# Kernel tuning notes

Hardware: AMD Instinct MI355X
Metric: run time of the kernel (lower is better)

Reference implementation:

```python
import jax, jax.numpy as jnp
import numpy as np
import math

N_RES, N_EDGE = 10000, 320000
C_S, C_Z, C_H, H, PQ, PV = 384, 128, 16, 12, 4, 8
INF, EPS = 1e5, 1e-8


def _lin(key, din, dout):
    k1, k2 = jax.random.split(key)
    w = jax.random.normal(k1, (din, dout), jnp.float32) * (1.0 / np.sqrt(din))
    b = jax.random.normal(k2, (dout,), jnp.float32) * 0.02
    return w, b


def setup_inputs() -> dict:
    key = jax.random.key(0)
    ks = jax.random.split(key, 16)
    s = jax.random.normal(ks[0], (N_RES, C_S), jnp.float32)
    z = jax.random.normal(ks[1], (N_EDGE, C_Z), jnp.float32)
    edge_index = jax.random.randint(ks[2], (2, N_EDGE), 0, N_RES, jnp.int32)
    rot = jnp.linalg.qr(jax.random.normal(ks[3], (N_RES, 3, 3), jnp.float32))[0]
    trans = jax.random.normal(ks[4], (N_RES, 3), jnp.float32)
    mask = jnp.ones((N_RES,), jnp.float32)
    wq, bq = _lin(ks[5], C_S, H * C_H)
    wkv, bkv = _lin(ks[6], C_S, 2 * H * C_H)
    wqp, bqp = _lin(ks[7], C_S, H * PQ * 3)
    wkvp, bkvp = _lin(ks[8], C_S, H * (PQ + PV) * 3)
    wb, bb = _lin(ks[9], C_Z, H)
    wdz, bdz = _lin(ks[10], C_Z, C_Z // 4)
    head_w = jax.random.normal(ks[11], (H,), jnp.float32) * 0.1
    wout, bout = _lin(ks[12], H * (C_Z // 4 + C_H + PV * 4), C_S)
    return dict(s=s, z=z, rot=rot, trans=trans, mask=mask, edge_index=edge_index,
                wq=wq, bq=bq, wkv=wkv, bkv=bkv, wqp=wqp, bqp=bqp, wkvp=wkvp, bkvp=bkvp,
                wb=wb, bb=bb, wdz=wdz, bdz=bdz, head_w=head_w, wout=wout, bout=bout)


def reference(s, z, rot, trans, mask, edge_index, wq, bq, wkv, bkv, wqp, bqp,
              wkvp, bkvp, wb, bb, wdz, bdz, head_w, wout, bout):
    n = s.shape[0]
    src, dst = edge_index[0], edge_index[1]  # key-side, query-side

    q = (s @ wq + bq).reshape(n, H, C_H)
    kv = (s @ wkv + bkv).reshape(n, H, 2 * C_H)
    k, v = kv[..., :C_H], kv[..., C_H:]

    def make_pts(x, p):
        # torch: split [n, H*p*3] into 3 chunks of H*p, stack on last dim -> [n, H*p, 3]
        x = jnp.stack(jnp.split(x, 3, axis=-1), axis=-1)
        x = jnp.einsum('nij,npj->npi', rot, x) + trans[:, None, :]  # global frame
        return x.reshape(n, H, p, 3)

    q_pts = make_pts(s @ wqp + bqp, PQ)                 # [n, H, PQ, 3]
    kv_pts = make_pts(s @ wkvp + bkvp, PQ + PV)
    k_pts, v_pts = kv_pts[..., :PQ, :], kv_pts[..., PQ:, :]

    b = z @ wb + bb                                      # [E, H]
    a = jnp.einsum('ehc,ehc->eh', q[dst], k[src]) * math.sqrt(1.0 / (3 * C_H))
    a = a + math.sqrt(1.0 / 3) * b

    disp = q_pts[dst] - k_pts[src]                       # [E, H, PQ, 3]
    hw = jax.nn.softplus(head_w) * math.sqrt(1.0 / (3 * (PQ * 9.0 / 2)))
    pt_att = -0.5 * jnp.einsum('ehp,h->eh', jnp.sum(disp * disp, axis=-1), hw)

    edge_mask = INF * (mask[src] * mask[dst] - 1.0)
    a = a + pt_att + edge_mask[:, None]

    # segment softmax over edges grouped by destination node
    m = jax.lax.stop_gradient(jax.ops.segment_max(a, dst, num_segments=n))
    ea = jnp.exp(a - m[dst])
    a = ea / (jax.ops.segment_sum(ea, dst, num_segments=n)[dst] + 1e-16)

    o = jax.ops.segment_sum(a[..., None] * v[src], dst, num_segments=n).reshape(n, -1)

    o_pt = jax.ops.segment_sum(a[..., None, None] * v_pts[src], dst, num_segments=n)  # [n,H,PV,3]
    o_pt = jnp.einsum('nji,nhpj->nhpi', rot, o_pt - trans[:, None, None, :])  # invert_apply
    o_pt_norm = jnp.sqrt(jnp.sum(o_pt * o_pt, axis=-1) + EPS).reshape(n, -1)
    o_pt = o_pt.reshape(n, H * PV, 3)

    pair_z = z @ wdz + bdz                               # [E, c_z//4]
    o_pair = jax.ops.segment_sum(a[..., None] * pair_z[:, None, :], dst,
                                 num_segments=n).reshape(n, -1)

    feats = jnp.concatenate([o, o_pt[..., 0], o_pt[..., 1], o_pt[..., 2],
                             o_pt_norm, o_pair], axis=-1)
    return feats @ wout + bout
```

## Files before the change

### kernel.cpp

```cpp
#include <hip/hip_runtime.h>
#include <hip/hip_bf16.h>
#include <math.h>

#define N_RESC 10000
#define N_EDGEC 320000
#define C_SC 384
#define C_ZC 128
#define AGG_D 864
#define FEAT_D 960
#define OUT_D 384

#define S1C 0.14433756729740643f
#define S2C 0.5773502691896258f
#define SHWC 0.13608276348795434f

__global__ void k_zero(int* cursor) {
    int i = blockIdx.x * 256 + threadIdx.x;
    if (i < N_RESC) cursor[i] = 0;
}

__global__ void k_hist(const int* __restrict__ ei, int* cursor) {
    int e = blockIdx.x * 256 + threadIdx.x;
    if (e < N_EDGEC) atomicAdd(&cursor[ei[N_EDGEC + e]], 1);
}

__global__ __launch_bounds__(1024) void k_scan(int* cursor, int* rowptr) {
    __shared__ int buf[1024];
    __shared__ int carry_s;
    int t = threadIdx.x;
    if (t == 0) carry_s = 0;
    __syncthreads();
    for (int ch = 0; ch < 10; ++ch) {
        int idx = ch * 1024 + t;
        int v = (idx < N_RESC) ? cursor[idx] : 0;
        buf[t] = v;
        __syncthreads();
        for (int off = 1; off < 1024; off <<= 1) {
            int x = (t >= off) ? buf[t - off] : 0;
            __syncthreads();
            buf[t] += x;
            __syncthreads();
        }
        int incl = buf[t];
        int excl = incl - v;
        int base = carry_s;
        int total = buf[1023];
        if (idx < N_RESC) { rowptr[idx] = base + excl; cursor[idx] = base + excl; }
        __syncthreads();
        if (t == 0) carry_s = base + total;
        __syncthreads();
    }
    if (t == 0) rowptr[N_RESC] = carry_s;
}

__global__ void k_scatter(const int* __restrict__ ei, int* cursor, int* csr,
                          int* src_csr, int* epos) {
    int e = blockIdx.x * 256 + threadIdx.x;
    if (e < N_EDGEC) {
        int d = ei[N_EDGEC + e];
        int s = ei[e];
        int pos = atomicAdd(&cursor[d], 1);
        csr[pos] = e;
        src_csr[pos] = s;
        epos[e] = pos;
    }
}

__global__ __launch_bounds__(256) void k_wpack(
    const float* __restrict__ wq, const float* __restrict__ bq,
    const float* __restrict__ wkv, const float* __restrict__ bkv,
    const float* __restrict__ wqp, const float* __restrict__ bqp,
    const float* __restrict__ wkvp, const float* __restrict__ bkvp,
    const float* __restrict__ wb, const float* __restrict__ bb,
    const float* __restrict__ wdz, const float* __restrict__ bdz,
    float* __restrict__ wpack, float* __restrict__ bpack,
    float* __restrict__ wzpack, float* __restrict__ bzpack) {
    int idx = blockIdx.x * 256 + threadIdx.x;
    if (idx < 384 * 1152) {
        int j = idx / 1152, c = idx % 1152;
        float v;
        if (c < 192)      v = wq[j * 192 + c];
        else if (c < 576) v = wkv[j * 384 + (c - 192)];
        else if (c < 720) v = wqp[j * 144 + (c - 576)];
        else              v = wkvp[j * 432 + (c - 720)];
        wpack[idx] = v;
    }
    if (idx < 1152) {
        float b;
        if (idx < 192)      b = bq[idx];
        else if (idx < 576) b = bkv[idx - 192];
        else if (idx < 720) b = bqp[idx - 576];
        else                b = bkvp[idx - 720];
        bpack[idx] = b;
    }
    if (idx < 128 * 48) {
        int j = idx / 48, c = idx % 48;
        float v = 0.f;
        if (c < 12)      v = wb[j * 12 + c];
        else if (c < 44) v = wdz[j * 32 + (c - 12)];
        wzpack[idx] = v;
    }
    if (idx < 48) {
        float b = 0.f;
        if (idx < 12)      b = bb[idx];
        else if (idx < 44) b = bdz[idx - 12];
        bzpack[idx] = b;
    }
}

#define BM 64
#define BN 128
#define BK 32
__global__ __launch_bounds__(256) void k_proj(const float* __restrict__ s,
    const float* __restrict__ wpack, const float* __restrict__ bpack,
    float* __restrict__ qh, float* __restrict__ kh, float* __restrict__ vh,
    float* __restrict__ praw) {
    __shared__ float sT[BK][BM + 4];
    __shared__ float wt[BK][BN];
    int t = threadIdx.x;
    int bm0 = blockIdx.x * BM;
    int bn0 = blockIdx.y * BN;
    int tcol = t & 31;
    int trow = t >> 5;
    int c0 = tcol * 4;
    int r0 = trow * 8;

    int srow = t >> 2;
    int skoff = (t & 3) * 8;
    int gsrow = min(bm0 + srow, N_RESC - 1);
    const float* srcp = s + (long)gsrow * C_SC + skoff;

    float acc[8][4];
    #pragma unroll
    for (int i = 0; i < 8; i++)
        #pragma unroll
        for (int j = 0; j < 4; j++) acc[i][j] = 0.f;

    for (int k0 = 0; k0 < C_SC; k0 += BK) {
        float4 sa = *(const float4*)(srcp + k0);
        float4 sb = *(const float4*)(srcp + k0 + 4);
        sT[skoff + 0][srow] = sa.x; sT[skoff + 1][srow] = sa.y;
        sT[skoff + 2][srow] = sa.z; sT[skoff + 3][srow] = sa.w;
        sT[skoff + 4][srow] = sb.x; sT[skoff + 5][srow] = sb.y;
        sT[skoff + 6][srow] = sb.z; sT[skoff + 7][srow] = sb.w;
        #pragma unroll
        for (int q = 0; q < 4; q++) {
            int kk = (t >> 5) + q * 8;
            *(float4*)&wt[kk][c0] =
                *(const float4*)(wpack + (long)(k0 + kk) * 1152 + bn0 + c0);
        }
        __syncthreads();
        #pragma unroll
        for (int k = 0; k < BK; k++) {
            float4 a0 = *(const float4*)&sT[k][r0];
            float4 a1 = *(const float4*)&sT[k][r0 + 4];
            float4 b  = *(const float4*)&wt[k][c0];
            float av0 = a0.x, av1 = a0.y, av2 = a0.z, av3 = a0.w;
            float av4 = a1.x, av5 = a1.y, av6 = a1.z, av7 = a1.w;
            acc[0][0] = fmaf(av0, b.x, acc[0][0]); acc[0][1] = fmaf(av0, b.y, acc[0][1]);
            acc[0][2] = fmaf(av0, b.z, acc[0][2]); acc[0][3] = fmaf(av0, b.w, acc[0][3]);
            acc[1][0] = fmaf(av1, b.x, acc[1][0]); acc[1][1] = fmaf(av1, b.y, acc[1][1]);
            acc[1][2] = fmaf(av1, b.z, acc[1][2]); acc[1][3] = fmaf(av1, b.w, acc[1][3]);
            acc[2][0] = fmaf(av2, b.x, acc[2][0]); acc[2][1] = fmaf(av2, b.y, acc[2][1]);
            acc[2][2] = fmaf(av2, b.z, acc[2][2]); acc[2][3] = fmaf(av2, b.w, acc[2][3]);
            acc[3][0] = fmaf(av3, b.x, acc[3][0]); acc[3][1] = fmaf(av3, b.y, acc[3][1]);
            acc[3][2] = fmaf(av3, b.z, acc[3][2]); acc[3][3] = fmaf(av3, b.w, acc[3][3]);
            acc[4][0] = fmaf(av4, b.x, acc[4][0]); acc[4][1] = fmaf(av4, b.y, acc[4][1]);
            acc[4][2] = fmaf(av4, b.z, acc[4][2]); acc[4][3] = fmaf(av4, b.w, acc[4][3]);
            acc[5][0] = fmaf(av5, b.x, acc[5][0]); acc[5][1] = fmaf(av5, b.y, acc[5][1]);
            acc[5][2] = fmaf(av5, b.z, acc[5][2]); acc[5][3] = fmaf(av5, b.w, acc[5][3]);
            acc[6][0] = fmaf(av6, b.x, acc[6][0]); acc[6][1] = fmaf(av6, b.y, acc[6][1]);
            acc[6][2] = fmaf(av6, b.z, acc[6][2]); acc[6][3] = fmaf(av6, b.w, acc[6][3]);
            acc[7][0] = fmaf(av7, b.x, acc[7][0]); acc[7][1] = fmaf(av7, b.y, acc[7][1]);
            acc[7][2] = fmaf(av7, b.z, acc[7][2]); acc[7][3] = fmaf(av7, b.w, acc[7][3]);
        }
        __syncthreads();
    }
    #pragma unroll
    for (int j = 0; j < 4; j++) {
        int c = bn0 + c0 + j;
        float bv = bpack[c];
        #pragma unroll
        for (int i = 0; i < 8; i++) {
            int n = bm0 + r0 + i;
            if (n < N_RESC) {
                float val = acc[i][j] + bv;
                if (c < 192) qh[(long)n * 192 + c] = val;
                else if (c < 576) {
                    int cc = c - 192; int h = cc >> 5, r = cc & 31;
                    if (r < 16) kh[(long)n * 192 + h * 16 + r] = val;
                    else        vh[(long)n * 192 + h * 16 + (r - 16)] = val;
                } else praw[(long)n * 576 + (c - 576)] = val;
            }
        }
    }
}

__global__ __launch_bounds__(192) void k_rot(const float* __restrict__ praw,
    const float* __restrict__ rot, const float* __restrict__ trans,
    float* __restrict__ qpts, float* __restrict__ kpts, float* __restrict__ vpts) {
    int n = blockIdx.x;
    int t = threadIdx.x;
    __shared__ float R[9], T[3];
    if (t < 9) R[t] = rot[n * 9 + t];
    if (t < 3) T[t] = trans[n * 3 + t];
    __syncthreads();
    const float* pr = praw + (long)n * 576;
    if (t < 48) {
        float x0 = pr[t], x1 = pr[48 + t], x2 = pr[96 + t];
        #pragma unroll
        for (int i = 0; i < 3; i++)
            qpts[(long)n * 144 + t * 3 + i] = R[i*3+0]*x0 + R[i*3+1]*x1 + R[i*3+2]*x2 + T[i];
    } else {
        int p = t - 48;
        float x0 = pr[144 + p], x1 = pr[288 + p], x2 = pr[432 + p];
        int h = p / 12, pp = p % 12;
        #pragma unroll
        for (int i = 0; i < 3; i++) {
            float val = R[i*3+0]*x0 + R[i*3+1]*x1 + R[i*3+2]*x2 + T[i];
            if (pp < 4) kpts[(long)n * 144 + (h * 4 + pp) * 3 + i] = val;
            else        vpts[(long)n * 288 + (h * 8 + (pp - 4)) * 3 + i] = val;
        }
    }
}

#define ZBM 128
__global__ __launch_bounds__(256) void k_zproj(const float* __restrict__ z,
    const int* __restrict__ epos,
    const float* __restrict__ wzpack, const float* __restrict__ bzpack,
    float* __restrict__ b_e, float* __restrict__ pairz) {
    __shared__ float zT[32][ZBM + 4];
    __shared__ float wl[128][48];
    int t = threadIdx.x;
    long e0 = (long)blockIdx.x * ZBM;
    int er = t & 31;
    int cg = t >> 5;
    int cb = cg * 6;

    #pragma unroll
    for (int q = 0; q < 6; q++) {
        int f = t + q * 256;
        int row = f / 12, c4 = f % 12;
        *(float4*)&wl[row][c4 * 4] = *(const float4*)(wzpack + row * 48 + c4 * 4);
    }

    float acc[4][6];
    #pragma unroll
    for (int i = 0; i < 4; i++)
        #pragma unroll
        for (int j = 0; j < 6; j++) acc[i][j] = 0.f;

    int r = t >> 1, ch2 = t & 1;
    const float* zp = z + (e0 + r) * C_ZC + ch2 * 16;

    for (int kc = 0; kc < 4; kc++) {
        __syncthreads();
        #pragma unroll
        for (int q = 0; q < 4; q++) {
            float4 v = *(const float4*)(zp + kc * 32 + q * 4);
            int kk = ch2 * 16 + q * 4;
            zT[kk + 0][r] = v.x; zT[kk + 1][r] = v.y;
            zT[kk + 2][r] = v.z; zT[kk + 3][r] = v.w;
        }
        __syncthreads();
        #pragma unroll
        for (int k = 0; k < 32; k++) {
            float4 zv = *(const float4*)&zT[k][er * 4];
            const float* wrow = &wl[kc * 32 + k][cb];
            float w0 = wrow[0], w1 = wrow[1], w2 = wrow[2];
            float w3 = wrow[3], w4 = wrow[4], w5 = wrow[5];
            acc[0][0] = fmaf(zv.x, w0, acc[0][0]); acc[0][1] = fmaf(zv.x, w1, acc[0][1]);
            acc[0][2] = fmaf(zv.x, w2, acc[0][2]); acc[0][3] = fmaf(zv.x, w3, acc[0][3]);
            acc[0][4] = fmaf(zv.x, w4, acc[0][4]); acc[0][5] = fmaf(zv.x, w5, acc[0][5]);
            acc[1][0] = fmaf(zv.y, w0, acc[1][0]); acc[1][1] = fmaf(zv.y, w1, acc[1][1]);
            acc[1][2] = fmaf(zv.y, w2, acc[1][2]); acc[1][3] = fmaf(zv.y, w3, acc[1][3]);
            acc[1][4] = fmaf(zv.y, w4, acc[1][4]); acc[1][5] = fmaf(zv.y, w5, acc[1][5]);
            acc[2][0] = fmaf(zv.z, w0, acc[2][0]); acc[2][1] = fmaf(zv.z, w1, acc[2][1]);
            acc[2][2] = fmaf(zv.z, w2, acc[2][2]); acc[2][3] = fmaf(zv.z, w3, acc[2][3]);
            acc[2][4] = fmaf(zv.z, w4, acc[2][4]); acc[2][5] = fmaf(zv.z, w5, acc[2][5]);
            acc[3][0] = fmaf(zv.w, w0, acc[3][0]); acc[3][1] = fmaf(zv.w, w1, acc[3][1]);
            acc[3][2] = fmaf(zv.w, w2, acc[3][2]); acc[3][3] = fmaf(zv.w, w3, acc[3][3]);
            acc[3][4] = fmaf(zv.w, w4, acc[3][4]); acc[3][5] = fmaf(zv.w, w5, acc[3][5]);
        }
    }

    float bz0 = bzpack[cb + 0], bz1 = bzpack[cb + 1], bz2 = bzpack[cb + 2];
    float bz3 = bzpack[cb + 3], bz4 = bzpack[cb + 4], bz5 = bzpack[cb + 5];
    #pragma unroll
    for (int ei = 0; ei < 4; ei++) {
        long pos = epos[e0 + er * 4 + ei];
        float o0 = acc[ei][0] + bz0, o1 = acc[ei][1] + bz1;
        float o2 = acc[ei][2] + bz2, o3 = acc[ei][3] + bz3;
        float o4 = acc[ei][4] + bz4, o5 = acc[ei][5] + bz5;
        if (cb < 12) {
            float* d = b_e + pos * 12 + cb;
            *(float2*)(d + 0) = make_float2(o0, o1);
            *(float2*)(d + 2) = make_float2(o2, o3);
            *(float2*)(d + 4) = make_float2(o4, o5);
        } else if (cb < 42) {
            float* d = pairz + pos * 32 + (cb - 12);
            *(float2*)(d + 0) = make_float2(o0, o1);
            *(float2*)(d + 2) = make_float2(o2, o3);
            *(float2*)(d + 4) = make_float2(o4, o5);
        } else {
            *(float2*)(pairz + pos * 32 + 30) = make_float2(o0, o1);
        }
    }
}

#define CAPL 256
__global__ __launch_bounds__(256) void k_logit(const int* __restrict__ rowptr,
    const int* __restrict__ src_csr,
    const float* __restrict__ qh, const float* __restrict__ kh,
    const float* __restrict__ qpts, const float* __restrict__ kpts,
    const float* __restrict__ mask, const float* __restrict__ head_w,
    const float* __restrict__ b_e, float* __restrict__ alog) {
    int n = blockIdx.x;
    int t = threadIdx.x;
    __shared__ float qf[192], qp[144], hws[12];
    __shared__ int slist[CAPL];
    if (t < 192) qf[t] = qh[(long)n * 192 + t];
    if (t < 144) qp[t] = qpts[(long)n * 144 + t];
    if (t < 12)  hws[t] = log1pf(expf(head_w[t])) * SHWC;
    float mdst = mask[n];
    int row0 = rowptr[n];
    int deg = rowptr[n + 1] - row0;
    int w = t >> 6, l = t & 63, c = l & 15, hq = l >> 4;
    for (int cs = 0; cs < deg; cs += CAPL) {
        int cnt = min(CAPL, deg - cs);
        __syncthreads();
        for (int i = t; i < cnt; i += 256) slist[i] = src_csr[row0 + cs + i];
        __syncthreads();
        for (int i = w * 2; i < cnt; i += 8) {
            int i1 = min(i + 1, cnt - 1);
            int s0 = slist[i], s1 = slist[i1];
            int pos0 = row0 + cs + i, pos1 = row0 + cs + i1;
            float em0 = 100000.0f * (mask[s0] * mdst - 1.0f);
            float em1 = 100000.0f * (mask[s1] * mdst - 1.0f);
            float kv0[3], kv1[3];
            #pragma unroll
            for (int tp = 0; tp < 3; tp++) {
                kv0[tp] = kh[(long)s0 * 192 + tp * 64 + l];
                kv1[tp] = kh[(long)s1 * 192 + tp * 64 + l];
            }
            float kp0[3] = {0.f,0.f,0.f}, kp1[3] = {0.f,0.f,0.f};
            if (c < 12) {
                #pragma unroll
                for (int tp = 0; tp < 3; tp++) {
                    int h = tp * 4 + hq;
                    kp0[tp] = kpts[(long)s0 * 144 + h * 12 + c];
                    kp1[tp] = kpts[(long)s1 * 144 + h * 12 + c];
                }
            }
            float be0[3] = {0.f,0.f,0.f}, be1[3] = {0.f,0.f,0.f};
            if (c == 0) {
                #pragma unroll
                for (int tp = 0; tp < 3; tp++) {
                    int h = tp * 4 + hq;
                    be0[tp] = b_e[(long)pos0 * 12 + h];
                    be1[tp] = b_e[(long)pos1 * 12 + h];
                }
            }
            #pragma unroll
            for (int tp = 0; tp < 3; tp++) {
                int h = tp * 4 + hq;
                float qfv = S1C * qf[h * 16 + c];
                float val0 = qfv * kv0[tp];
                float val1 = qfv * kv1[tp];
                if (c < 12) {
                    float qpv = qp[h * 12 + c];
                    float hw = -0.5f * hws[h];
                    float d0 = qpv - kp0[tp];
                    float d1 = qpv - kp1[tp];
                    val0 = fmaf(hw * d0, d0, val0);
                    val1 = fmaf(hw * d1, d1, val1);
                }
                val0 += __shfl_xor(val0, 8, 16); val1 += __shfl_xor(val1, 8, 16);
                val0 += __shfl_xor(val0, 4, 16); val1 += __shfl_xor(val1, 4, 16);
                val0 += __shfl_xor(val0, 2, 16); val1 += __shfl_xor(val1, 2, 16);
                val0 += __shfl_xor(val0, 1, 16); val1 += __shfl_xor(val1, 1, 16);
                if (c == 0) {
                    alog[(long)pos0 * 12 + h] = val0 + S2C * be0[tp] + em0;
                    if (i1 != i)
                        alog[(long)pos1 * 12 + h] = val1 + S2C * be1[tp] + em1;
                }
            }
        }
    }
}

#define CAPE 256
__global__ __launch_bounds__(256) void k_agg(const int* __restrict__ rowptr,
    const int* __restrict__ src_csr,
    const float* __restrict__ alog, const float* __restrict__ vh,
    const float* __restrict__ vpts, const float* __restrict__ pairz,
    float* __restrict__ agg) {
    int n = blockIdx.x;
    int t = threadIdx.x;
    __shared__ float red[16 * 12];
    __shared__ float mh[12], linv[12];
    __shared__ float al[CAPE * 12];
    __shared__ int sl_[CAPE];
    int row0 = rowptr[n];
    int deg = rowptr[n + 1] - row0;
    int g = t >> 4, l16 = t & 15;
    if (l16 < 12) {
        float lm = -1e30f;
        for (int i = g; i < deg; i += 16)
            lm = fmaxf(lm, alog[(long)(row0 + i) * 12 + l16]);
        red[g * 12 + l16] = lm;
    }
    __syncthreads();
    if (t < 12) {
        float m = -1e30f;
        for (int gg = 0; gg < 16; gg++) m = fmaxf(m, red[gg * 12 + t]);
        mh[t] = m;
    }
    __syncthreads();
    if (l16 < 12) {
        float m = mh[l16];
        float ls = 0.f;
        for (int i = g; i < deg; i += 16)
            ls += expf(alog[(long)(row0 + i) * 12 + l16] - m);
        red[g * 12 + l16] = ls;
    }
    __syncthreads();
    if (t < 12) {
        float ssum = 0.f;
        for (int gg = 0; gg < 16; gg++) ssum += red[gg * 12 + t];
        linv[t] = 1.f / (ssum + 1e-16f);
    }

    const float* base = nullptr;
    int scale = 0, hk = 0, use_e = 0;
    int comp = t * 4;
    if (comp < 192)      { base = vh + comp; scale = 192; hk = comp >> 4; }
    else if (comp < 480) { int idx = comp - 192; base = vpts + idx; scale = 288; hk = idx / 24; }
    else if (comp < 864) { int idx = comp - 480; base = pairz + (idx & 31); scale = 32; hk = idx >> 5; use_e = 1; }
    float4 acc = make_float4(0.f, 0.f, 0.f, 0.f);

    for (int cs = 0; cs < deg; cs += CAPE) {
        int cnt = min(CAPE, deg - cs);
        int p0 = row0 + cs;
        __syncthreads();
        for (int i = t; i < cnt * 12; i += 256) {
            int h = i % 12;
            al[i] = expf(alog[(long)p0 * 12 + i] - mh[h]) * linv[h];
        }
        for (int i = t; i < cnt; i += 256) sl_[i] = src_csr[p0 + i];
        __syncthreads();
        if (t < 216) {
            int i = 0;
            for (; i + 4 <= cnt; i += 4) {
                int i0 = use_e ? (p0 + i)     : sl_[i];
                int i1 = use_e ? (p0 + i + 1) : sl_[i+1];
                int i2 = use_e ? (p0 + i + 2) : sl_[i+2];
                int i3 = use_e ? (p0 + i + 3) : sl_[i+3];
                float4 v0 = *(const float4*)(base + (long)i0 * scale);
                float4 v1 = *(const float4*)(base + (long)i1 * scale);
                float4 v2 = *(const float4*)(base + (long)i2 * scale);
                float4 v3 = *(const float4*)(base + (long)i3 * scale);
                float w0 = al[i * 12 + hk];
                float w1 = al[(i+1) * 12 + hk];
                float w2 = al[(i+2) * 12 + hk];
                float w3 = al[(i+3) * 12 + hk];
                acc.x = fmaf(w0, v0.x, acc.x); acc.y = fmaf(w0, v0.y, acc.y);
                acc.z = fmaf(w0, v0.z, acc.z); acc.w = fmaf(w0, v0.w, acc.w);
                acc.x = fmaf(w1, v1.x, acc.x); acc.y = fmaf(w1, v1.y, acc.y);
                acc.z = fmaf(w1, v1.z, acc.z); acc.w = fmaf(w1, v1.w, acc.w);
                acc.x = fmaf(w2, v2.x, acc.x); acc.y = fmaf(w2, v2.y, acc.y);
                acc.z = fmaf(w2, v2.z, acc.z); acc.w = fmaf(w2, v2.w, acc.w);
                acc.x = fmaf(w3, v3.x, acc.x); acc.y = fmaf(w3, v3.y, acc.y);
                acc.z = fmaf(w3, v3.z, acc.z); acc.w = fmaf(w3, v3.w, acc.w);
            }
            for (; i < cnt; i++) {
                int ii = use_e ? (p0 + i) : sl_[i];
                float4 v = *(const float4*)(base + (long)ii * scale);
                float w = al[i * 12 + hk];
                acc.x = fmaf(w, v.x, acc.x); acc.y = fmaf(w, v.y, acc.y);
                acc.z = fmaf(w, v.z, acc.z); acc.w = fmaf(w, v.w, acc.w);
            }
        }
    }
    if (t < 216) *(float4*)(agg + (long)n * AGG_D + comp) = acc;
}

#define NT_F 8
__global__ __launch_bounds__(192) void k_final(const float* __restrict__ agg,
    const float* __restrict__ rot, const float* __restrict__ trans,
    const float* __restrict__ wout, const float* __restrict__ bout,
    float* __restrict__ out) {
    __shared__ float f[NT_F][FEAT_D];
    int t = threadIdx.x;
    int node0 = blockIdx.x * NT_F;
    for (int idx = t; idx < NT_F * 192; idx += 192) {
        int nt = idx / 192, c = idx % 192;
        f[nt][c] = agg[(long)(node0 + nt) * AGG_D + c];
    }
    for (int idx = t; idx < NT_F * 96; idx += 192) {
        int nt = idx / 96, p = idx % 96;
        int n = node0 + nt;
        const float* a = agg + (long)n * AGG_D;
        float gx = a[192 + p * 3 + 0] - trans[n * 3 + 0];
        float gy = a[192 + p * 3 + 1] - trans[n * 3 + 1];
        float gz = a[192 + p * 3 + 2] - trans[n * 3 + 2];
        const float* R = rot + (long)n * 9;
        float lx = R[0] * gx + R[3] * gy + R[6] * gz;
        float ly = R[1] * gx + R[4] * gy + R[7] * gz;
        float lz = R[2] * gx + R[5] * gy + R[8] * gz;
        f[nt][192 + p] = lx;
        f[nt][288 + p] = ly;
        f[nt][384 + p] = lz;
        f[nt][480 + p] = sqrtf(lx * lx + ly * ly + lz * lz + 1e-8f);
    }
    for (int idx = t; idx < NT_F * 384; idx += 192) {
        int nt = idx / 384, q = idx % 384;
        f[nt][576 + q] = agg[(long)(node0 + nt) * AGG_D + 480 + q];
    }
    __syncthreads();
    float acc0[NT_F], acc1[NT_F];
    float b0 = bout[t], b1 = bout[t + 192];
    #pragma unroll
    for (int nt = 0; nt < NT_F; nt++) { acc0[nt] = b0; acc1[nt] = b1; }
    for (int j = 0; j < FEAT_D; j += 4) {
        float4 fv[NT_F];
        #pragma unroll
        for (int nt = 0; nt < NT_F; nt++) fv[nt] = *(const float4*)&f[nt][j];
        #pragma unroll
        for (int u = 0; u < 4; u++) {
            float w0 = wout[(j + u) * OUT_D + t];
            float w1 = wout[(j + u) * OUT_D + t + 192];
            #pragma unroll
            for (int nt = 0; nt < NT_F; nt++) {
                float fvu = (u == 0) ? fv[nt].x : (u == 1) ? fv[nt].y : (u == 2) ? fv[nt].z : fv[nt].w;
                acc0[nt] = fmaf(fvu, w0, acc0[nt]);
                acc1[nt] = fmaf(fvu, w1, acc1[nt]);
            }
        }
    }
    #pragma unroll
    for (int nt = 0; nt < NT_F; nt++) {
        out[(long)(node0 + nt) * OUT_D + t] = acc0[nt];
        out[(long)(node0 + nt) * OUT_D + t + 192] = acc1[nt];
    }
}

extern "C" void kernel_launch(void* const* d_in, const int* in_sizes, int n_in,
                              void* d_out, int out_size, void* d_ws, size_t ws_size,
                              hipStream_t stream) {
    const float* s     = (const float*)d_in[0];
    const float* z     = (const float*)d_in[1];
    const float* rot   = (const float*)d_in[2];
    const float* trans = (const float*)d_in[3];
    const float* mask  = (const float*)d_in[4];
    const int*   ei    = (const int*)d_in[5];
    const float* wq    = (const float*)d_in[6];
    const float* bq    = (const float*)d_in[7];
    const float* wkv   = (const float*)d_in[8];
    const float* bkv   = (const float*)d_in[9];
    const float* wqp   = (const float*)d_in[10];
    const float* bqp   = (const float*)d_in[11];
    const float* wkvp  = (const float*)d_in[12];
    const float* bkvp  = (const float*)d_in[13];
    const float* wb    = (const float*)d_in[14];
    const float* bb    = (const float*)d_in[15];
    const float* wdz   = (const float*)d_in[16];
    const float* bdz   = (const float*)d_in[17];
    const float* head_w= (const float*)d_in[18];
    const float* wout  = (const float*)d_in[19];
    const float* bout  = (const float*)d_in[20];
    float* out = (float*)d_out;

    float* ws    = (float*)d_ws;
    float* qh    = ws;
    float* kh    = qh + 1920000;
    float* vh    = kh + 1920000;
    float* qpts  = vh + 1920000;
    float* kpts  = qpts + 1440000;
    float* vpts  = kpts + 1440000;
    float* b_e   = vpts + 2880000;
    float* pairz = b_e + 3840000;
    float* alog  = pairz + 10240000;
    float* agg   = alog + 3840000;
    float* praw  = agg;
    float* wpack = agg + 5760000;
    float* bpack = wpack + 442368;
    float* wzpack= bpack + 1152;
    float* bzpack= wzpack + 6144;
    int* rowptr  = (int*)(agg + 8640000);
    int* cursor  = rowptr + 10004;
    int* csr     = cursor + 10000;
    int* src_csr = csr + N_EDGEC;
    int* epos    = src_csr + N_EDGEC;

    k_zero<<<(N_RESC + 255) / 256, 256, 0, stream>>>(cursor);
    k_hist<<<(N_EDGEC + 255) / 256, 256, 0, stream>>>(ei, cursor);
    k_scan<<<1, 1024, 0, stream>>>(cursor, rowptr);
    k_scatter<<<(N_EDGEC + 255) / 256, 256, 0, stream>>>(ei, cursor, csr, src_csr, epos);

    k_wpack<<<(384 * 1152 + 255) / 256, 256, 0, stream>>>(wq, bq, wkv, bkv, wqp, bqp,
                                                          wkvp, bkvp, wb, bb, wdz, bdz,
                                                          wpack, bpack, wzpack, bzpack);
    dim3 pgrid((N_RESC + BM - 1) / BM, 1152 / BN);
    k_proj<<<pgrid, 256, 0, stream>>>(s, wpack, bpack, qh, kh, vh, praw);
    k_rot<<<N_RESC, 192, 0, stream>>>(praw, rot, trans, qpts, kpts, vpts);

    k_zproj<<<N_EDGEC / ZBM, 256, 0, stream>>>(z, epos, wzpack, bzpack, b_e, pairz);

    k_logit<<<N_RESC, 256, 0, stream>>>(rowptr, src_csr, qh, kh, qpts, kpts,
                                        mask, head_w, b_e, alog);

    k_agg<<<N_RESC, 256, 0, stream>>>(rowptr, src_csr, alog, vh, vpts, pairz, agg);

    k_final<<<N_RESC / NT_F, 192, 0, stream>>>(agg, rot, trans, wout, bout, out);
}
```

Before: 800.8 us.

## Split final projection into feature-assembly kernel and tiled shared-memory GEMM

The fused final kernel, which built features in shared memory and then ran a naive per-thread GEMM over 8 nodes, is split in two. The first kernel writes the 960-wide feature rows to a workspace buffer that reuses the pairz region. The second kernel runs a register-blocked tiled GEMM, reusing the BM/BN/BK tiling from the projection kernel, so each weight tile is loaded once per 8x4 register tile. The aim is to cut redundant global reads of the weights and raise FMA throughput, at the cost of one extra kernel launch and a round trip of the feature matrix through global memory.

```diff
diff --git a/kernel.cpp b/kernel.cpp
--- a/kernel.cpp
+++ b/kernel.cpp
@@ -486,16 +486,14 @@
 }
 
 #define NT_F 8
-__global__ __launch_bounds__(192) void k_final(const float* __restrict__ agg,
+__global__ __launch_bounds__(192) void k_feat(const float* __restrict__ agg,
     const float* __restrict__ rot, const float* __restrict__ trans,
-    const float* __restrict__ wout, const float* __restrict__ bout,
-    float* __restrict__ out) {
-    __shared__ float f[NT_F][FEAT_D];
+    float* __restrict__ feats) {
     int t = threadIdx.x;
     int node0 = blockIdx.x * NT_F;
     for (int idx = t; idx < NT_F * 192; idx += 192) {
         int nt = idx / 192, c = idx % 192;
-        f[nt][c] = agg[(long)(node0 + nt) * AGG_D + c];
+        feats[(long)(node0 + nt) * FEAT_D + c] = agg[(long)(node0 + nt) * AGG_D + c];
     }
     for (int idx = t; idx < NT_F * 96; idx += 192) {
         int nt = idx / 96, p = idx % 96;
@@ -508,40 +506,95 @@
         float lx = R[0] * gx + R[3] * gy + R[6] * gz;
         float ly = R[1] * gx + R[4] * gy + R[7] * gz;
         float lz = R[2] * gx + R[5] * gy + R[8] * gz;
-        f[nt][192 + p] = lx;
-        f[nt][288 + p] = ly;
-        f[nt][384 + p] = lz;
-        f[nt][480 + p] = sqrtf(lx * lx + ly * ly + lz * lz + 1e-8f);
+        float* f = feats + (long)n * FEAT_D;
+        f[192 + p] = lx;
+        f[288 + p] = ly;
+        f[384 + p] = lz;
+        f[480 + p] = sqrtf(lx * lx + ly * ly + lz * lz + 1e-8f);
     }
     for (int idx = t; idx < NT_F * 384; idx += 192) {
         int nt = idx / 384, q = idx % 384;
-        f[nt][576 + q] = agg[(long)(node0 + nt) * AGG_D + 480 + q];
-    }
-    __syncthreads();
-    float acc0[NT_F], acc1[NT_F];
-    float b0 = bout[t], b1 = bout[t + 192];
+        feats[(long)(node0 + nt) * FEAT_D + 576 + q] =
+            agg[(long)(node0 + nt) * AGG_D + 480 + q];
+    }
+}
+
+__global__ __launch_bounds__(256) void k_out(const float* __restrict__ feats,
+    const float* __restrict__ wout, const float* __restrict__ bout,
+    float* __restrict__ out) {
+    __shared__ float sT[BK][BM + 4];
+    __shared__ float wt[BK][BN];
+    int t = threadIdx.x;
+    int bm0 = blockIdx.x * BM;
+    int bn0 = blockIdx.y * BN;
+    int tcol = t & 31;
+    int trow = t >> 5;
+    int c0 = tcol * 4;
+    int r0 = trow * 8;
+
+    int srow = t >> 2;
+    int skoff = (t & 3) * 8;
+    int gsrow = min(bm0 + srow, N_RESC - 1);
+    const float* srcp = feats + (long)gsrow * FEAT_D + skoff;
+
+    float acc[8][4];
     #pragma unroll
-    for (int nt = 0; nt < NT_F; nt++) { acc0[nt] = b0; acc1[nt] = b1; }
-    for (int j = 0; j < FEAT_D; j += 4) {
-        float4 fv[NT_F];
-        #pragma unroll
-        for (int nt = 0; nt < NT_F; nt++) fv[nt] = *(const float4*)&f[nt][j];
-        #pragma unroll
-        for (int u = 0; u < 4; u++) {
-            float w0 = wout[(j + u) * OUT_D + t];
-            float w1 = wout[(j + u) * OUT_D + t + 192];
-            #pragma unroll
-            for (int nt = 0; nt < NT_F; nt++) {
-                float fvu = (u == 0) ? fv[nt].x : (u == 1) ? fv[nt].y : (u == 2) ? fv[nt].z : fv[nt].w;
-                acc0[nt] = fmaf(fvu, w0, acc0[nt]);
-                acc1[nt] = fmaf(fvu, w1, acc1[nt]);
-            }
-        }
-    }
+    for (int i = 0; i < 8; i++)
+        #pragma unroll
+        for (int j = 0; j < 4; j++) acc[i][j] = 0.f;
+
+    for (int k0 = 0; k0 < FEAT_D; k0 += BK) {
+        float4 sa = *(const float4*)(srcp + k0);
+        float4 sb = *(const float4*)(srcp + k0 + 4);
+        sT[skoff + 0][srow] = sa.x; sT[skoff + 1][srow] = sa.y;
+        sT[skoff + 2][srow] = sa.z; sT[skoff + 3][srow] = sa.w;
+        sT[skoff + 4][srow] = sb.x; sT[skoff + 5][srow] = sb.y;
+        sT[skoff + 6][srow] = sb.z; sT[skoff + 7][srow] = sb.w;
+        #pragma unroll
+        for (int q = 0; q < 4; q++) {
+            int kk = (t >> 5) + q * 8;
+            *(float4*)&wt[kk][c0] =
+                *(const float4*)(wout + (long)(k0 + kk) * OUT_D + bn0 + c0);
+        }
+        __syncthreads();
+        #pragma unroll
+        for (int k = 0; k < BK; k++) {
+            float4 a0 = *(const float4*)&sT[k][r0];
+            float4 a1 = *(const float4*)&sT[k][r0 + 4];
+            float4 b  = *(const float4*)&wt[k][c0];
+            float av0 = a0.x, av1 = a0.y, av2 = a0.z, av3 = a0.w;
+            float av4 = a1.x, av5 = a1.y, av6 = a1.z, av7 = a1.w;
+            acc[0][0] = fmaf(av0, b.x, acc[0][0]); acc[0][1] = fmaf(av0, b.y, acc[0][1]);
+            acc[0][2] = fmaf(av0, b.z, acc[0][2]); acc[0][3] = fmaf(av0, b.w, acc[0][3]);
+            acc[1][0] = fmaf(av1, b.x, acc[1][0]); acc[1][1] = fmaf(av1, b.y, acc[1][1]);
+            acc[1][2] = fmaf(av1, b.z, acc[1][2]); acc[1][3] = fmaf(av1, b.w, acc[1][3]);
+            acc[2][0] = fmaf(av2, b.x, acc[2][0]); acc[2][1] = fmaf(av2, b.y, acc[2][1]);
+            acc[2][2] = fmaf(av2, b.z, acc[2][2]); acc[2][3] = fmaf(av2, b.w, acc[2][3]);
+            acc[3][0] = fmaf(av3, b.x, acc[3][0]); acc[3][1] = fmaf(av3, b.y, acc[3][1]);
+            acc[3][2] = fmaf(av3, b.z, acc[3][2]); acc[3][3] = fmaf(av3, b.w, acc[3][3]);
+            acc[4][0] = fmaf(av4, b.x, acc[4][0]); acc[4][1] = fmaf(av4, b.y, acc[4][1]);
+            acc[4][2] = fmaf(av4, b.z, acc[4][2]); acc[4][3] = fmaf(av4, b.w, acc[4][3]);
+            acc[5][0] = fmaf(av5, b.x, acc[5][0]); acc[5][1] = fmaf(av5, b.y, acc[5][1]);
+            acc[5][2] = fmaf(av5, b.z, acc[5][2]); acc[5][3] = fmaf(av5, b.w, acc[5][3]);
+            acc[6][0] = fmaf(av6, b.x, acc[6][0]); acc[6][1] = fmaf(av6, b.y, acc[6][1]);
+            acc[6][2] = fmaf(av6, b.z, acc[6][2]); acc[6][3] = fmaf(av6, b.w, acc[6][3]);
+            acc[7][0] = fmaf(av7, b.x, acc[7][0]); acc[7][1] = fmaf(av7, b.y, acc[7][1]);
+            acc[7][2] = fmaf(av7, b.z, acc[7][2]); acc[7][3] = fmaf(av7, b.w, acc[7][3]);
+        }
+        __syncthreads();
+    }
+    float bv0 = bout[bn0 + c0 + 0];
+    float bv1 = bout[bn0 + c0 + 1];
+    float bv2 = bout[bn0 + c0 + 2];
+    float bv3 = bout[bn0 + c0 + 3];
     #pragma unroll
-    for (int nt = 0; nt < NT_F; nt++) {
-        out[(long)(node0 + nt) * OUT_D + t] = acc0[nt];
-        out[(long)(node0 + nt) * OUT_D + t + 192] = acc1[nt];
+    for (int i = 0; i < 8; i++) {
+        int n = bm0 + r0 + i;
+        if (n < N_RESC) {
+            *(float4*)(out + (long)n * OUT_D + bn0 + c0) =
+                make_float4(acc[i][0] + bv0, acc[i][1] + bv1,
+                            acc[i][2] + bv2, acc[i][3] + bv3);
+        }
     }
 }
 
@@ -587,6 +640,7 @@
     float* bpack = wpack + 442368;
     float* wzpack= bpack + 1152;
     float* bzpack= wzpack + 6144;
+    float* feats = pairz;
     int* rowptr  = (int*)(agg + 8640000);
     int* cursor  = rowptr + 10004;
     int* csr     = cursor + 10000;
@@ -612,5 +666,7 @@
 
     k_agg<<<N_RESC, 256, 0, stream>>>(rowptr, src_csr, alog, vh, vpts, pairz, agg);
 
-    k_final<<<N_RESC / NT_F, 192, 0, stream>>>(agg, rot, trans, wout, bout, out);
-}
+    k_feat<<<N_RESC / NT_F, 192, 0, stream>>>(agg, rot, trans, feats);
+    dim3 ogrid((N_RESC + BM - 1) / BM, OUT_D / BN);
+    k_out<<<ogrid, 256, 0, stream>>>(feats, wout, bout, out);
+}
```

New measurement: 768.5 us. 1.04x faster.
